# Optimization experiments

Measured on AMD Instinct MI355X. Metric: run time of the kernel, lower is better.

The kernel has to match this reference:

```python
import jax, jax.numpy as jnp
import numpy as np
from jax import lax

NUM_KERNELS = 256
B, C, L = 128, 10, 16384
EPS = 1e-10
NORMALIZE = True
KERNEL_LENGTHS = np.array([7, 9, 11])


def _make_kernel_meta():
    """Deterministic ROCKET-style ragged kernel metadata (static ints)."""
    rng = np.random.default_rng(0)
    lengths = rng.choice(KERNEL_LENGTHS, NUM_KERNELS).astype(np.int64)
    nci = rng.integers(1, C + 1, NUM_KERNELS).astype(np.int64)  # channels per kernel
    channel_indices = np.concatenate(
        [rng.choice(C, int(n), replace=False) for n in nci]).astype(np.int64)
    dilations = np.array(
        [int(2 ** rng.uniform(0.0, np.log2((L - 1) / (l - 1)))) for l in lengths],
        dtype=np.int64)
    paddings = np.array(
        [((l - 1) * d) // 2 if rng.integers(2) else 0 for l, d in zip(lengths, dilations)],
        dtype=np.int64)
    return lengths, nci, channel_indices, dilations, paddings


def setup_inputs() -> dict:
    lengths, nci, channel_indices, dilations, paddings = _make_kernel_meta()
    total_w = int(np.sum(lengths * nci))
    key = jax.random.key(0)
    kx, kw, kb = jax.random.split(key, 3)
    x = jax.random.normal(kx, (B, C, L), dtype=jnp.float32)
    weights = jax.random.normal(kw, (total_w,), dtype=jnp.float32)
    biases = jax.random.uniform(kb, (NUM_KERNELS,), minval=-1.0, maxval=1.0,
                                dtype=jnp.float32)
    return {
        'x': x,
        'weights': weights,
        'biases': biases,
        'lengths': jnp.asarray(lengths),
        'dilations': jnp.asarray(dilations),
        'paddings': jnp.asarray(paddings),
        'num_channel_indices': jnp.asarray(nci),
        'channel_indices': jnp.asarray(channel_indices),
    }


def reference(x, weights, biases, lengths, dilations, paddings,
              num_channel_indices, channel_indices):
    # Ragged metadata must be static (defines per-kernel shapes).
    lengths = np.asarray(lengths)
    dilations = np.asarray(dilations)
    paddings = np.asarray(paddings)
    nci = np.asarray(num_channel_indices)
    channel_indices = np.asarray(channel_indices)
    windices = np.concatenate([[0], np.cumsum(lengths * nci)])
    cindices = np.concatenate([[0], np.cumsum(nci)])

    if NORMALIZE:
        mean_ = jnp.mean(x, axis=-1, keepdims=True)
        std_ = jnp.std(x, axis=-1, keepdims=True, ddof=1)  # torch unbiased std
        x = (x - mean_) / (std_ + EPS)

    ppvs, mxs = [], []
    for k in range(NUM_KERNELS):
        w = weights[windices[k]:windices[k + 1]].reshape(int(nci[k]), int(lengths[k]))
        chans = channel_indices[cindices[k]:cindices[k + 1]]
        px = x[:, chans, :]                       # [B, c_k, L]
        d, p = int(dilations[k]), int(paddings[k])
        yy = lax.conv_general_dilated(
            px, w[None],                          # rhs: [1, c_k, len_k]
            window_strides=(1,), padding=[(p, p)], rhs_dilation=(d,),
            dimension_numbers=('NCH', 'OIH', 'NCH'))[:, 0, :] + biases[k]  # [B, Lout]
        ppvs.append(jnp.mean((yy > 0).astype(x.dtype), axis=-1))
        sm = jax.nn.softmax(yy * 1000.0, axis=-1)  # sharp softmax ~ smooth max
        mxs.append(jnp.sum(sm * yy, axis=-1))

    ppv = jnp.stack(ppvs, axis=1)                 # [B, K]
    mx = jnp.stack(mxs, axis=1)                   # [B, K]
    # interleave: y[:, 2k] = ppv_k, y[:, 2k+1] = mx_k
    return jnp.stack([ppv, mx], axis=2).reshape(x.shape[0], 2 * NUM_KERNELS)
```

## Files before the change

### kernel.cpp

```cpp
#include <hip/hip_runtime.h>

#define NK 256
#define BB 128
#define CC 10
#define LL 16384
#define EPSV 1e-10f
#define GS2 15
#define XW 1792
#define WROW 12

__device__ __forceinline__ void block_finish(int cnt, float mx,
                                             float* rm, int* rc,
                                             int Lout, float* out, int b, int k) {
    int tid = threadIdx.x;
    for (int off = 32; off; off >>= 1) {
        mx = fmaxf(mx, __shfl_down(mx, off));
        cnt += __shfl_down(cnt, off);
    }
    int wv = tid >> 6, ln = tid & 63;
    if (ln == 0) { rm[wv] = mx; rc[wv] = cnt; }
    __syncthreads();
    if (tid == 0) {
#pragma unroll
        for (int i = 1; i < 4; ++i) { mx = fmaxf(mx, rm[i]); cnt += rc[i]; }
        size_t o = (size_t)b * (2 * NK) + 2 * k;
        out[o] = (float)cnt / (float)Lout;
        out[o + 1] = mx;
    }
}

__global__ __launch_bounds__(256) void stats_kernel(const float* __restrict__ x,
                                                    float* __restrict__ wsf) {
    int row = blockIdx.x;
    const float4* x4 = (const float4*)(x + (size_t)row * LL);
    int tid = threadIdx.x;
    float s = 0.f, s2 = 0.f;
    for (int i = tid; i < LL / 4; i += 256) {
        float4 v = x4[i];
        s += v.x + v.y + v.z + v.w;
        s2 += v.x * v.x + v.y * v.y + v.z * v.z + v.w * v.w;
    }
    for (int off = 32; off; off >>= 1) {
        s += __shfl_down(s, off);
        s2 += __shfl_down(s2, off);
    }
    __shared__ float as_[4], as2_[4];
    int wv = tid >> 6, ln = tid & 63;
    if (ln == 0) { as_[wv] = s; as2_[wv] = s2; }
    __syncthreads();
    if (tid == 0) {
        float S = as_[0] + as_[1] + as_[2] + as_[3];
        float S2 = as2_[0] + as2_[1] + as2_[2] + as2_[3];
        float mean = S / (float)LL;
        float var = (S2 - (float)LL * mean * mean) / (float)(LL - 1);
        var = fmaxf(var, 0.f);
        float inv = 1.f / (sqrtf(var) + EPSV);
        wsf[row] = inv;
        wsf[1280 + row] = -mean * inv;
    }
}

__global__ __launch_bounds__(256) void prefix_kernel(const int* __restrict__ lengths,
                                                     const int* __restrict__ ncis,
                                                     int* __restrict__ wbase,
                                                     int* __restrict__ cbase) {
    __shared__ int s1[NK], s2[NK];
    int k = threadIdx.x;
    int v1 = lengths[k] * ncis[k];
    int v2 = ncis[k];
    s1[k] = v1; s2[k] = v2;
    for (int off = 1; off < NK; off <<= 1) {
        __syncthreads();
        int a = (k >= off) ? s1[k - off] : 0;
        int b = (k >= off) ? s2[k - off] : 0;
        __syncthreads();
        s1[k] += a; s2[k] += b;
    }
    __syncthreads();
    wbase[k] = s1[k] - v1;
    cbase[k] = s2[k] - v2;
}

template <int LEN>
__device__ __forceinline__ void conv_S(
    const float* __restrict__ x, float* __restrict__ xw,
    const float* __restrict__ wsmR, const float* __restrict__ wsmS,
    const int* __restrict__ choff, const float* __restrict__ cinv,
    const float* __restrict__ csh,
    int d, int ms, int Lout, int nci, float biasE, float biasI,
    int wu, int lane, int& cnt, float& mx) {
    constexpr int W = GS2 + LEN - 1;
    const int qpt = 64 / d;
    const int MT = qpt * GS2;
    const int stot = d * (MT + LEN - 1);
    const int nit4 = (stot + 3 + 255) >> 8;
    const int nitS = (stot + 3 + 63) >> 6;
    const int Qmax = (Lout + d - 1) / d;
    const int nqt = (Qmax + MT - 1) / MT;
    int qi = lane / d, rho = lane - qi * d;
    bool act = qi < qpt;
    int a0 = act ? qi * GS2 * d + rho : 0;
    float rv[28];

    for (int j = wu; j < nqt; j += 4) {
        int qt = j * MT;
        int tb = (qt - ms) * d;
        int off = tb & 3, base = tb - off;
        bool interior = (base >= 0) && (base + (nit4 << 8) <= LL);
        float acc[GS2];
#pragma unroll
        for (int g = 0; g < GS2; ++g) acc[g] = 0.f;

        if (interior) {
            {
                const float* xp = x + choff[0] + base + 4 * lane;
#pragma unroll
                for (int it = 0; it < 7; ++it)
                    if (it < nit4) *(float4*)&rv[4 * it] = *(const float4*)(xp + (it << 8));
            }
            for (int ci = 0; ci < nci; ++ci) {
#pragma unroll
                for (int it = 0; it < 7; ++it)
                    if (it < nit4) *(float4*)&xw[4 * lane + (it << 8)] = *(const float4*)&rv[4 * it];
                if (ci + 1 < nci) {
                    const float* xp = x + choff[ci + 1] + base + 4 * lane;
#pragma unroll
                    for (int it = 0; it < 7; ++it)
                        if (it < nit4) *(float4*)&rv[4 * it] = *(const float4*)(xp + (it << 8));
                }
                float wreg[WROW];
                const float4* wv4 = (const float4*)&wsmS[ci * WROW];
#pragma unroll
                for (int u = 0; u < (LEN + 3) / 4; ++u) {
                    float4 w4 = wv4[u];
                    wreg[4 * u + 0] = w4.x; wreg[4 * u + 1] = w4.y;
                    wreg[4 * u + 2] = w4.z; wreg[4 * u + 3] = w4.w;
                }
                float win[W];
                int a = off + a0;
#pragma unroll
                for (int i = 0; i < W; ++i) { win[i] = xw[a]; a += d; }
                __builtin_amdgcn_s_setprio(1);
#pragma unroll
                for (int jj = 0; jj < LEN; ++jj)
#pragma unroll
                    for (int g = 0; g < GS2; ++g)
                        acc[g] = fmaf(wreg[jj], win[g + jj], acc[g]);
                __builtin_amdgcn_s_setprio(0);
            }
        } else {
            {
                const float* xc = x + choff[0];
#pragma unroll
                for (int it = 0; it < 26; ++it)
                    if (it < nitS) {
                        int t = base + (it << 6) + lane;
                        t = t < 0 ? 0 : (t > LL - 1 ? LL - 1 : t);
                        rv[it] = xc[t];
                    }
            }
            for (int ci = 0; ci < nci; ++ci) {
                float inv = cinv[ci], sh = csh[ci];
#pragma unroll
                for (int it = 0; it < 26; ++it)
                    if (it < nitS) {
                        int t = base + (it << 6) + lane;
                        float v = ((unsigned)t < (unsigned)LL) ? fmaf(rv[it], inv, sh) : 0.f;
                        xw[(it << 6) + lane] = v;
                    }
                if (ci + 1 < nci) {
                    const float* xc = x + choff[ci + 1];
#pragma unroll
                    for (int it = 0; it < 26; ++it)
                        if (it < nitS) {
                            int t = base + (it << 6) + lane;
                            t = t < 0 ? 0 : (t > LL - 1 ? LL - 1 : t);
                            rv[it] = xc[t];
                        }
                }
                float wreg[WROW];
                const float4* wv4 = (const float4*)&wsmR[ci * WROW];
#pragma unroll
                for (int u = 0; u < (LEN + 3) / 4; ++u) {
                    float4 w4 = wv4[u];
                    wreg[4 * u + 0] = w4.x; wreg[4 * u + 1] = w4.y;
                    wreg[4 * u + 2] = w4.z; wreg[4 * u + 3] = w4.w;
                }
                float win[W];
                int a = off + a0;
#pragma unroll
                for (int i = 0; i < W; ++i) { win[i] = xw[a]; a += d; }
                __builtin_amdgcn_s_setprio(1);
#pragma unroll
                for (int jj = 0; jj < LEN; ++jj)
#pragma unroll
                    for (int g = 0; g < GS2; ++g)
                        acc[g] = fmaf(wreg[jj], win[g + jj], acc[g]);
                __builtin_amdgcn_s_setprio(0);
            }
        }

        float bt = interior ? biasI : biasE;
        if (act) {
            int qb = qt + qi * GS2;
            if ((qb + GS2) * d <= Lout) {
                float am = acc[0];
#pragma unroll
                for (int g = 1; g < GS2; ++g) am = fmaxf(am, acc[g]);
                mx = fmaxf(mx, am + bt);
                float nb = -bt;
#pragma unroll
                for (int g = 0; g < GS2; ++g) cnt += (acc[g] > nb) ? 1 : 0;
            } else {
#pragma unroll
                for (int g = 0; g < GS2; ++g) {
                    int t = (qb + g) * d + rho;
                    if (t < Lout) {
                        float y = acc[g] + bt;
                        cnt += (y > 0.f) ? 1 : 0;
                        mx = fmaxf(mx, y);
                    }
                }
            }
        }
    }
}

template <int LEN, int GG>
__device__ __forceinline__ void conv_T(
    const float* __restrict__ x,
    const float* __restrict__ wsmR, const float* __restrict__ wsmS,
    const int* __restrict__ choff, const float* __restrict__ cinv,
    const float* __restrict__ csh,
    int d, int ms, int Lout, int nci, float biasE, float biasI,
    int wu, int lane, int& cnt, float& mx) {
    constexpr int M = GG + LEN - 1;
    const int Qmax = (Lout + d - 1) / d;
    const int nqt = (Qmax + GG - 1) / GG;
    const int NT = d * nqt;

    for (int f0 = wu * 64; f0 < NT; f0 += 256) {
        int f = f0 + lane;
        bool active = f < NT;
        int fc = active ? f : NT - 1;
        unsigned qi = (unsigned)fc / (unsigned)d;
        int rho = fc - (int)qi * d;
        int qb0 = (int)qi * GG;
        int tl = (qb0 - ms) * d + rho;
        bool laneInt = (tl >= 0) && (tl + (M - 1) * d < LL);
        bool interior = __all(laneInt);
        float acc[GG];
#pragma unroll
        for (int g = 0; g < GG; ++g) acc[g] = 0.f;

        float rA[M], rB[M];

        if (interior) {
            {
                const float* xc = x + choff[0];
                int t = tl;
#pragma unroll
                for (int m = 0; m < M; ++m) { rA[m] = xc[t]; t += d; }
            }
            int ci = 0;
            while (true) {
                if (ci + 1 < nci) {
                    const float* xc = x + choff[ci + 1];
                    int t = tl;
#pragma unroll
                    for (int m = 0; m < M; ++m) { rB[m] = xc[t]; t += d; }
                }
                {
                    float wreg[WROW];
                    const float4* wv4 = (const float4*)&wsmS[ci * WROW];
#pragma unroll
                    for (int u = 0; u < (LEN + 3) / 4; ++u) {
                        float4 w4 = wv4[u];
                        wreg[4 * u + 0] = w4.x; wreg[4 * u + 1] = w4.y;
                        wreg[4 * u + 2] = w4.z; wreg[4 * u + 3] = w4.w;
                    }
                    __builtin_amdgcn_s_setprio(1);
#pragma unroll
                    for (int jj = 0; jj < LEN; ++jj)
#pragma unroll
                        for (int g = 0; g < GG; ++g)
                            acc[g] = fmaf(wreg[jj], rA[g + jj], acc[g]);
                    __builtin_amdgcn_s_setprio(0);
                }
                ++ci; if (ci >= nci) break;
                if (ci + 1 < nci) {
                    const float* xc = x + choff[ci + 1];
                    int t = tl;
#pragma unroll
                    for (int m = 0; m < M; ++m) { rA[m] = xc[t]; t += d; }
                }
                {
                    float wreg[WROW];
                    const float4* wv4 = (const float4*)&wsmS[ci * WROW];
#pragma unroll
                    for (int u = 0; u < (LEN + 3) / 4; ++u) {
                        float4 w4 = wv4[u];
                        wreg[4 * u + 0] = w4.x; wreg[4 * u + 1] = w4.y;
                        wreg[4 * u + 2] = w4.z; wreg[4 * u + 3] = w4.w;
                    }
                    __builtin_amdgcn_s_setprio(1);
#pragma unroll
                    for (int jj = 0; jj < LEN; ++jj)
#pragma unroll
                        for (int g = 0; g < GG; ++g)
                            acc[g] = fmaf(wreg[jj], rB[g + jj], acc[g]);
                    __builtin_amdgcn_s_setprio(0);
                }
                ++ci; if (ci >= nci) break;
            }
        } else {
            {
                const float* xc = x + choff[0];
                int t = tl;
#pragma unroll
                for (int m = 0; m < M; ++m) {
                    int tc = t < 0 ? 0 : (t > LL - 1 ? LL - 1 : t);
                    rA[m] = xc[tc]; t += d;
                }
            }
            int ci = 0;
            while (true) {
                if (ci + 1 < nci) {
                    const float* xc = x + choff[ci + 1];
                    int t = tl;
#pragma unroll
                    for (int m = 0; m < M; ++m) {
                        int tc = t < 0 ? 0 : (t > LL - 1 ? LL - 1 : t);
                        rB[m] = xc[tc]; t += d;
                    }
                }
                {
                    float inv = cinv[ci], sh = csh[ci];
                    int t = tl;
#pragma unroll
                    for (int m = 0; m < M; ++m) {
                        rA[m] = ((unsigned)t < (unsigned)LL) ? fmaf(rA[m], inv, sh) : 0.f;
                        t += d;
                    }
                    float wreg[WROW];
                    const float4* wv4 = (const float4*)&wsmR[ci * WROW];
#pragma unroll
                    for (int u = 0; u < (LEN + 3) / 4; ++u) {
                        float4 w4 = wv4[u];
                        wreg[4 * u + 0] = w4.x; wreg[4 * u + 1] = w4.y;
                        wreg[4 * u + 2] = w4.z; wreg[4 * u + 3] = w4.w;
                    }
                    __builtin_amdgcn_s_setprio(1);
#pragma unroll
                    for (int jj = 0; jj < LEN; ++jj)
#pragma unroll
                        for (int g = 0; g < GG; ++g)
                            acc[g] = fmaf(wreg[jj], rA[g + jj], acc[g]);
                    __builtin_amdgcn_s_setprio(0);
                }
                ++ci; if (ci >= nci) break;
                if (ci + 1 < nci) {
                    const float* xc = x + choff[ci + 1];
                    int t = tl;
#pragma unroll
                    for (int m = 0; m < M; ++m) {
                        int tc = t < 0 ? 0 : (t > LL - 1 ? LL - 1 : t);
                        rA[m] = xc[tc]; t += d;
                    }
                }
                {
                    float inv = cinv[ci], sh = csh[ci];
                    int t = tl;
#pragma unroll
                    for (int m = 0; m < M; ++m) {
                        rB[m] = ((unsigned)t < (unsigned)LL) ? fmaf(rB[m], inv, sh) : 0.f;
                        t += d;
                    }
                    float wreg[WROW];
                    const float4* wv4 = (const float4*)&wsmR[ci * WROW];
#pragma unroll
                    for (int u = 0; u < (LEN + 3) / 4; ++u) {
                        float4 w4 = wv4[u];
                        wreg[4 * u + 0] = w4.x; wreg[4 * u + 1] = w4.y;
                        wreg[4 * u + 2] = w4.z; wreg[4 * u + 3] = w4.w;
                    }
                    __builtin_amdgcn_s_setprio(1);
#pragma unroll
                    for (int jj = 0; jj < LEN; ++jj)
#pragma unroll
                        for (int g = 0; g < GG; ++g)
                            acc[g] = fmaf(wreg[jj], rB[g + jj], acc[g]);
                    __builtin_amdgcn_s_setprio(0);
                }
                ++ci; if (ci >= nci) break;
            }
        }

        float bt = interior ? biasI : biasE;
        if (active) {
            if ((qb0 + GG) * d <= Lout) {
                float am = acc[0];
#pragma unroll
                for (int g = 1; g < GG; ++g) am = fmaxf(am, acc[g]);
                mx = fmaxf(mx, am + bt);
                float nb = -bt;
#pragma unroll
                for (int g = 0; g < GG; ++g) cnt += (acc[g] > nb) ? 1 : 0;
            } else {
#pragma unroll
                for (int g = 0; g < GG; ++g) {
                    int t = (qb0 + g) * d + rho;
                    if (t < Lout) {
                        float y = acc[g] + bt;
                        cnt += (y > 0.f) ? 1 : 0;
                        mx = fmaxf(mx, y);
                    }
                }
            }
        }
    }
}

__global__ __launch_bounds__(256) void conv_kernel(
    const float* __restrict__ x, const float* __restrict__ weights,
    const float* __restrict__ biases,
    const int* __restrict__ lengths, const int* __restrict__ dil,
    const int* __restrict__ pad, const int* __restrict__ ncis,
    const int* __restrict__ chidx,
    const float* __restrict__ wsf, const int* __restrict__ wbase,
    const int* __restrict__ cbase, float* __restrict__ out) {
    int k = blockIdx.x, b = blockIdx.y;
    __shared__ __align__(16) float xl[4 * XW];
    __shared__ __align__(16) float wsmR[CC * WROW];
    __shared__ __align__(16) float wsmS[CC * WROW];
    __shared__ int choff[CC];
    __shared__ float cinv[CC], csh[CC];
    __shared__ float rm[4];
    __shared__ int rc[4];

    int tid = threadIdx.x;
    int len = lengths[k], d = dil[k], p = pad[k], nci = ncis[k];
    int wb = wbase[k], cb = cbase[k];

    if (tid < nci) {
        int ch = chidx[cb + tid];
        choff[tid] = (b * CC + ch) * LL;
        cinv[tid] = wsf[b * CC + ch];
        csh[tid] = wsf[1280 + b * CC + ch];
    }
    __syncthreads();
    for (int i = tid; i < nci * WROW; i += 256) {
        int ci = i / WROW, jj = i - ci * WROW;
        float wv = (jj < len) ? weights[wb + ci * len + jj] : 0.f;
        wsmR[i] = wv;
        wsmS[i] = wv * cinv[ci];
    }
    __syncthreads();

    float csum = 0.f;
    for (int ci = 0; ci < nci; ++ci) {
        float sw = 0.f;
        for (int jj = 0; jj < WROW; ++jj) sw += wsmR[ci * WROW + jj];
        csum += csh[ci] * sw;
    }

    int span = (len - 1) * d;
    int Lout = LL + 2 * p - span;
    int ms = p / d;
    float biasE = biases[k];
    float biasI = biasE + csum;
    int Qmax = (Lout + d - 1) / d;

    int wu = tid >> 6;
    int lane = tid & 63;
    float* xw = xl + wu * XW;
    int cnt = 0;
    float mx = -3.4e38f;

    if (d <= 64) {
        switch (len) {
            case 7:  conv_S<7>(x, xw, wsmR, wsmS, choff, cinv, csh, d, ms, Lout, nci, biasE, biasI, wu, lane, cnt, mx); break;
            case 9:  conv_S<9>(x, xw, wsmR, wsmS, choff, cinv, csh, d, ms, Lout, nci, biasE, biasI, wu, lane, cnt, mx); break;
            default: conv_S<11>(x, xw, wsmR, wsmS, choff, cinv, csh, d, ms, Lout, nci, biasE, biasI, wu, lane, cnt, mx); break;
        }
    } else if (Qmax > 12) {
        switch (len) {
            case 7:  conv_T<7, 16>(x, wsmR, wsmS, choff, cinv, csh, d, ms, Lout, nci, biasE, biasI, wu, lane, cnt, mx); break;
            case 9:  conv_T<9, 16>(x, wsmR, wsmS, choff, cinv, csh, d, ms, Lout, nci, biasE, biasI, wu, lane, cnt, mx); break;
            default: conv_T<11, 16>(x, wsmR, wsmS, choff, cinv, csh, d, ms, Lout, nci, biasE, biasI, wu, lane, cnt, mx); break;
        }
    } else {
        switch (len) {
            case 7:  conv_T<7, 4>(x, wsmR, wsmS, choff, cinv, csh, d, ms, Lout, nci, biasE, biasI, wu, lane, cnt, mx); break;
            case 9:  conv_T<9, 4>(x, wsmR, wsmS, choff, cinv, csh, d, ms, Lout, nci, biasE, biasI, wu, lane, cnt, mx); break;
            default: conv_T<11, 4>(x, wsmR, wsmS, choff, cinv, csh, d, ms, Lout, nci, biasE, biasI, wu, lane, cnt, mx); break;
        }
    }
    block_finish(cnt, mx, rm, rc, Lout, out, b, k);
}

extern "C" void kernel_launch(void* const* d_in, const int* in_sizes, int n_in,
                              void* d_out, int out_size, void* d_ws, size_t ws_size,
                              hipStream_t stream) {
    const float* x = (const float*)d_in[0];
    const float* weights = (const float*)d_in[1];
    const float* biases = (const float*)d_in[2];
    const int* lengths = (const int*)d_in[3];
    const int* dil = (const int*)d_in[4];
    const int* pad = (const int*)d_in[5];
    const int* ncis = (const int*)d_in[6];
    const int* chidx = (const int*)d_in[7];
    float* out = (float*)d_out;

    float* wsf = (float*)d_ws;
    int* wbase = (int*)((char*)d_ws + 2560 * sizeof(float));
    int* cbase = wbase + NK;

    stats_kernel<<<dim3(BB * CC), dim3(256), 0, stream>>>(x, wsf);
    prefix_kernel<<<dim3(1), dim3(256), 0, stream>>>(lengths, ncis, wbase, cbase);
    dim3 grid(NK, BB);
    conv_kernel<<<grid, dim3(256), 0, stream>>>(x, weights, biases, lengths, dil,
                                                pad, ncis, chidx, wsf, wbase,
                                                cbase, out);
}
```

Before: 2.322 ms.

## Deepen prefetch pipeline across tiles and channels, shrink per-thread output groups

conv_S is restructured into a flat software pipeline over (tile, channel) pairs with two register buffers, so loads for the next channel or next tile are issued before the current compute, including across tile boundaries. conv_T's interior path gains triple buffering, prefetching two channels ahead. Output group sizes shrink (GS2 15->11, GG 16->12) along with the LDS window, which lowers register pressure and makes room for the extra buffers. The trade-off is more tiles, each with more halo overhead, in exchange for better latency hiding and possibly higher occupancy.

```diff
diff --git a/kernel.cpp b/kernel.cpp
--- a/kernel.cpp
+++ b/kernel.cpp
@@ -5,8 +5,8 @@
 #define CC 10
 #define LL 16384
 #define EPSV 1e-10f
-#define GS2 15
-#define XW 1792
+#define GS2 11
+#define XW 1536
 #define WROW 12
 
 __device__ __forceinline__ void block_finish(int cnt, float mx,
@@ -100,109 +100,74 @@
     int qi = lane / d, rho = lane - qi * d;
     bool act = qi < qpt;
     int a0 = act ? qi * GS2 * d + rho : 0;
-    float rv[28];
-
-    for (int j = wu; j < nqt; j += 4) {
-        int qt = j * MT;
-        int tb = (qt - ms) * d;
-        int off = tb & 3, base = tb - off;
-        bool interior = (base >= 0) && (base + (nit4 << 8) <= LL);
-        float acc[GS2];
-#pragma unroll
-        for (int g = 0; g < GS2; ++g) acc[g] = 0.f;
-
-        if (interior) {
-            {
-                const float* xp = x + choff[0] + base + 4 * lane;
-#pragma unroll
-                for (int it = 0; it < 7; ++it)
-                    if (it < nit4) *(float4*)&rv[4 * it] = *(const float4*)(xp + (it << 8));
-            }
-            for (int ci = 0; ci < nci; ++ci) {
-#pragma unroll
-                for (int it = 0; it < 7; ++it)
-                    if (it < nit4) *(float4*)&xw[4 * lane + (it << 8)] = *(const float4*)&rv[4 * it];
-                if (ci + 1 < nci) {
-                    const float* xp = x + choff[ci + 1] + base + 4 * lane;
-#pragma unroll
-                    for (int it = 0; it < 7; ++it)
-                        if (it < nit4) *(float4*)&rv[4 * it] = *(const float4*)(xp + (it << 8));
-                }
-                float wreg[WROW];
-                const float4* wv4 = (const float4*)&wsmS[ci * WROW];
-#pragma unroll
-                for (int u = 0; u < (LEN + 3) / 4; ++u) {
-                    float4 w4 = wv4[u];
-                    wreg[4 * u + 0] = w4.x; wreg[4 * u + 1] = w4.y;
-                    wreg[4 * u + 2] = w4.z; wreg[4 * u + 3] = w4.w;
-                }
-                float win[W];
-                int a = off + a0;
-#pragma unroll
-                for (int i = 0; i < W; ++i) { win[i] = xw[a]; a += d; }
-                __builtin_amdgcn_s_setprio(1);
-#pragma unroll
-                for (int jj = 0; jj < LEN; ++jj)
-#pragma unroll
-                    for (int g = 0; g < GS2; ++g)
-                        acc[g] = fmaf(wreg[jj], win[g + jj], acc[g]);
-                __builtin_amdgcn_s_setprio(0);
-            }
+
+    float rvA[24], rvB[24];
+
+    auto tbOf = [&](int j) { return (j * MT - ms) * d; };
+    auto isInt = [&](int tb_) {
+        int base = tb_ - (tb_ & 3);
+        return (base >= 0) && (base + (nit4 << 8) <= LL);
+    };
+    auto pref = [&](float (&rv)[24], int c, int tb_) {
+        int base = tb_ - (tb_ & 3);
+        const float* xc = x + choff[c];
+        if (isInt(tb_)) {
+            const float* xp = xc + base + 4 * lane;
+#pragma unroll
+            for (int it = 0; it < 6; ++it)
+                if (it < nit4) *(float4*)&rv[4 * it] = *(const float4*)(xp + (it << 8));
         } else {
-            {
-                const float* xc = x + choff[0];
-#pragma unroll
-                for (int it = 0; it < 26; ++it)
-                    if (it < nitS) {
-                        int t = base + (it << 6) + lane;
-                        t = t < 0 ? 0 : (t > LL - 1 ? LL - 1 : t);
-                        rv[it] = xc[t];
-                    }
-            }
-            for (int ci = 0; ci < nci; ++ci) {
-                float inv = cinv[ci], sh = csh[ci];
-#pragma unroll
-                for (int it = 0; it < 26; ++it)
-                    if (it < nitS) {
-                        int t = base + (it << 6) + lane;
-                        float v = ((unsigned)t < (unsigned)LL) ? fmaf(rv[it], inv, sh) : 0.f;
-                        xw[(it << 6) + lane] = v;
-                    }
-                if (ci + 1 < nci) {
-                    const float* xc = x + choff[ci + 1];
-#pragma unroll
-                    for (int it = 0; it < 26; ++it)
-                        if (it < nitS) {
-                            int t = base + (it << 6) + lane;
-                            t = t < 0 ? 0 : (t > LL - 1 ? LL - 1 : t);
-                            rv[it] = xc[t];
-                        }
-                }
-                float wreg[WROW];
-                const float4* wv4 = (const float4*)&wsmR[ci * WROW];
-#pragma unroll
-                for (int u = 0; u < (LEN + 3) / 4; ++u) {
-                    float4 w4 = wv4[u];
-                    wreg[4 * u + 0] = w4.x; wreg[4 * u + 1] = w4.y;
-                    wreg[4 * u + 2] = w4.z; wreg[4 * u + 3] = w4.w;
-                }
-                float win[W];
-                int a = off + a0;
-#pragma unroll
-                for (int i = 0; i < W; ++i) { win[i] = xw[a]; a += d; }
-                __builtin_amdgcn_s_setprio(1);
-#pragma unroll
-                for (int jj = 0; jj < LEN; ++jj)
-#pragma unroll
-                    for (int g = 0; g < GS2; ++g)
-                        acc[g] = fmaf(wreg[jj], win[g + jj], acc[g]);
-                __builtin_amdgcn_s_setprio(0);
-            }
-        }
-
-        float bt = interior ? biasI : biasE;
+#pragma unroll
+            for (int it = 0; it < 22; ++it)
+                if (it < nitS) {
+                    int t = base + (it << 6) + lane;
+                    t = t < 0 ? 0 : (t > LL - 1 ? LL - 1 : t);
+                    rv[it] = xc[t];
+                }
+        }
+    };
+    auto wstage = [&](float (&rv)[24], int tb_, float inv, float sh) {
+        int base = tb_ - (tb_ & 3);
+        if (isInt(tb_)) {
+#pragma unroll
+            for (int it = 0; it < 6; ++it)
+                if (it < nit4) *(float4*)&xw[4 * lane + (it << 8)] = *(const float4*)&rv[4 * it];
+        } else {
+#pragma unroll
+            for (int it = 0; it < 22; ++it)
+                if (it < nitS) {
+                    int t = base + (it << 6) + lane;
+                    float v = ((unsigned)t < (unsigned)LL) ? fmaf(rv[it], inv, sh) : 0.f;
+                    xw[(it << 6) + lane] = v;
+                }
+        }
+    };
+    auto compute = [&](int cc, bool I, int off, float (&acc)[GS2]) {
+        const float* wt = I ? wsmS : wsmR;
+        float wreg[WROW];
+        const float4* wv4 = (const float4*)&wt[cc * WROW];
+#pragma unroll
+        for (int u = 0; u < (LEN + 3) / 4; ++u) {
+            float4 w4 = wv4[u];
+            wreg[4 * u + 0] = w4.x; wreg[4 * u + 1] = w4.y;
+            wreg[4 * u + 2] = w4.z; wreg[4 * u + 3] = w4.w;
+        }
+        float win[W];
+        int a = off + a0;
+#pragma unroll
+        for (int i = 0; i < W; ++i) { win[i] = xw[a]; a += d; }
+        __builtin_amdgcn_s_setprio(1);
+#pragma unroll
+        for (int jj = 0; jj < LEN; ++jj)
+#pragma unroll
+            for (int g = 0; g < GS2; ++g)
+                acc[g] = fmaf(wreg[jj], win[g + jj], acc[g]);
+        __builtin_amdgcn_s_setprio(0);
+    };
+    auto epilogue = [&](int jc, bool I, float (&acc)[GS2]) {
+        float bt = I ? biasI : biasE;
         if (act) {
-            int qb = qt + qi * GS2;
+            int qb = jc * MT + qi * GS2;
             if ((qb + GS2) * d <= Lout) {
                 float am = acc[0];
 #pragma unroll
@@ -222,6 +187,47 @@
                     }
                 }
             }
+        }
+    };
+
+    int jc = wu, cc = 0;
+    int jp = wu, cp = 0;
+    auto adv = [&]() { ++cp; if (cp == nci) { cp = 0; jp += 4; } };
+
+    if (jc >= nqt) return;
+
+    pref(rvA, cp, tbOf(jp)); adv();
+    if (jp < nqt) { pref(rvB, cp, tbOf(jp)); adv(); }
+
+    float acc[GS2];
+#pragma unroll
+    for (int g = 0; g < GS2; ++g) acc[g] = 0.f;
+    int tb = tbOf(jc); int off = tb & 3; bool I = isInt(tb);
+
+    while (true) {
+        wstage(rvA, tb, cinv[cc], csh[cc]);
+        if (jp < nqt) { pref(rvA, cp, tbOf(jp)); adv(); }
+        compute(cc, I, off, acc);
+        ++cc;
+        if (cc == nci) {
+            epilogue(jc, I, acc);
+            cc = 0; jc += 4;
+            if (jc >= nqt) break;
+#pragma unroll
+            for (int g = 0; g < GS2; ++g) acc[g] = 0.f;
+            tb = tbOf(jc); off = tb & 3; I = isInt(tb);
+        }
+        wstage(rvB, tb, cinv[cc], csh[cc]);
+        if (jp < nqt) { pref(rvB, cp, tbOf(jp)); adv(); }
+        compute(cc, I, off, acc);
+        ++cc;
+        if (cc == nci) {
+            epilogue(jc, I, acc);
+            cc = 0; jc += 4;
+            if (jc >= nqt) break;
+#pragma unroll
+            for (int g = 0; g < GS2; ++g) acc[g] = 0.f;
+            tb = tbOf(jc); off = tb & 3; I = isInt(tb);
         }
     }
 }
@@ -253,145 +259,76 @@
 #pragma unroll
         for (int g = 0; g < GG; ++g) acc[g] = 0.f;
 
-        float rA[M], rB[M];
+        float rA[M], rB[M], rC[M];
+
+        auto fmaW = [&](float (&r)[M], int c, const float* wt) {
+            float wreg[WROW];
+            const float4* wv4 = (const float4*)&wt[c * WROW];
+#pragma unroll
+            for (int u = 0; u < (LEN + 3) / 4; ++u) {
+                float4 w4 = wv4[u];
+                wreg[4 * u + 0] = w4.x; wreg[4 * u + 1] = w4.y;
+                wreg[4 * u + 2] = w4.z; wreg[4 * u + 3] = w4.w;
+            }
+            __builtin_amdgcn_s_setprio(1);
+#pragma unroll
+            for (int jj = 0; jj < LEN; ++jj)
+#pragma unroll
+                for (int g = 0; g < GG; ++g)
+                    acc[g] = fmaf(wreg[jj], r[g + jj], acc[g]);
+            __builtin_amdgcn_s_setprio(0);
+        };
 
         if (interior) {
-            {
-                const float* xc = x + choff[0];
+            auto ldI = [&](float (&r)[M], int c) {
+                const float* xc = x + choff[c];
                 int t = tl;
 #pragma unroll
-                for (int m = 0; m < M; ++m) { rA[m] = xc[t]; t += d; }
-            }
+                for (int m = 0; m < M; ++m) { r[m] = xc[t]; t += d; }
+            };
+            ldI(rA, 0);
+            if (nci > 1) ldI(rB, 1);
             int ci = 0;
             while (true) {
-                if (ci + 1 < nci) {
-                    const float* xc = x + choff[ci + 1];
-                    int t = tl;
-#pragma unroll
-                    for (int m = 0; m < M; ++m) { rB[m] = xc[t]; t += d; }
-                }
-                {
-                    float wreg[WROW];
-                    const float4* wv4 = (const float4*)&wsmS[ci * WROW];
-#pragma unroll
-                    for (int u = 0; u < (LEN + 3) / 4; ++u) {
-                        float4 w4 = wv4[u];
-                        wreg[4 * u + 0] = w4.x; wreg[4 * u + 1] = w4.y;
-                        wreg[4 * u + 2] = w4.z; wreg[4 * u + 3] = w4.w;
-                    }
-                    __builtin_amdgcn_s_setprio(1);
-#pragma unroll
-                    for (int jj = 0; jj < LEN; ++jj)
-#pragma unroll
-                        for (int g = 0; g < GG; ++g)
-                            acc[g] = fmaf(wreg[jj], rA[g + jj], acc[g]);
-                    __builtin_amdgcn_s_setprio(0);
-                }
+                if (ci + 2 < nci) ldI(rC, ci + 2);
+                fmaW(rA, ci, wsmS);
                 ++ci; if (ci >= nci) break;
-                if (ci + 1 < nci) {
-                    const float* xc = x + choff[ci + 1];
-                    int t = tl;
-#pragma unroll
-                    for (int m = 0; m < M; ++m) { rA[m] = xc[t]; t += d; }
-                }
-                {
-                    float wreg[WROW];
-                    const float4* wv4 = (const float4*)&wsmS[ci * WROW];
-#pragma unroll
-                    for (int u = 0; u < (LEN + 3) / 4; ++u) {
-                        float4 w4 = wv4[u];
-                        wreg[4 * u + 0] = w4.x; wreg[4 * u + 1] = w4.y;
-                        wreg[4 * u + 2] = w4.z; wreg[4 * u + 3] = w4.w;
-                    }
-                    __builtin_amdgcn_s_setprio(1);
-#pragma unroll
-                    for (int jj = 0; jj < LEN; ++jj)
-#pragma unroll
-                        for (int g = 0; g < GG; ++g)
-                            acc[g] = fmaf(wreg[jj], rB[g + jj], acc[g]);
-                    __builtin_amdgcn_s_setprio(0);
-                }
+                if (ci + 2 < nci) ldI(rA, ci + 2);
+                fmaW(rB, ci, wsmS);
+                ++ci; if (ci >= nci) break;
+                if (ci + 2 < nci) ldI(rB, ci + 2);
+                fmaW(rC, ci, wsmS);
                 ++ci; if (ci >= nci) break;
             }
         } else {
-            {
-                const float* xc = x + choff[0];
+            auto ldE = [&](float (&r)[M], int c) {
+                const float* xc = x + choff[c];
                 int t = tl;
 #pragma unroll
                 for (int m = 0; m < M; ++m) {
                     int tc = t < 0 ? 0 : (t > LL - 1 ? LL - 1 : t);
-                    rA[m] = xc[tc]; t += d;
-                }
-            }
+                    r[m] = xc[tc]; t += d;
+                }
+            };
+            auto nrm = [&](float (&r)[M], int c) {
+                float inv = cinv[c], sh = csh[c];
+                int t = tl;
+#pragma unroll
+                for (int m = 0; m < M; ++m) {
+                    r[m] = ((unsigned)t < (unsigned)LL) ? fmaf(r[m], inv, sh) : 0.f;
+                    t += d;
+                }
+            };
+            ldE(rA, 0);
             int ci = 0;
             while (true) {
-                if (ci + 1 < nci) {
-                    const float* xc = x + choff[ci + 1];
-                    int t = tl;
-#pragma unroll
-                    for (int m = 0; m < M; ++m) {
-                        int tc = t < 0 ? 0 : (t > LL - 1 ? LL - 1 : t);
-                        rB[m] = xc[tc]; t += d;
-                    }
-                }
-                {
-                    float inv = cinv[ci], sh = csh[ci];
-                    int t = tl;
-#pragma unroll
-                    for (int m = 0; m < M; ++m) {
-                        rA[m] = ((unsigned)t < (unsigned)LL) ? fmaf(rA[m], inv, sh) : 0.f;
-                        t += d;
-                    }
-                    float wreg[WROW];
-                    const float4* wv4 = (const float4*)&wsmR[ci * WROW];
-#pragma unroll
-                    for (int u = 0; u < (LEN + 3) / 4; ++u) {
-                        float4 w4 = wv4[u];
-                        wreg[4 * u + 0] = w4.x; wreg[4 * u + 1] = w4.y;
-                        wreg[4 * u + 2] = w4.z; wreg[4 * u + 3] = w4.w;
-                    }
-                    __builtin_amdgcn_s_setprio(1);
-#pragma unroll
-                    for (int jj = 0; jj < LEN; ++jj)
-#pragma unroll
-                        for (int g = 0; g < GG; ++g)
-                            acc[g] = fmaf(wreg[jj], rA[g + jj], acc[g]);
-                    __builtin_amdgcn_s_setprio(0);
-                }
+                if (ci + 1 < nci) ldE(rB, ci + 1);
+                nrm(rA, ci);
+                fmaW(rA, ci, wsmR);
                 ++ci; if (ci >= nci) break;
-                if (ci + 1 < nci) {
-                    const float* xc = x + choff[ci + 1];
-                    int t = tl;
-#pragma unroll
-                    for (int m = 0; m < M; ++m) {
-                        int tc = t < 0 ? 0 : (t > LL - 1 ? LL - 1 : t);
-                        rA[m] = xc[tc]; t += d;
-                    }
-                }
-                {
-                    float inv = cinv[ci], sh = csh[ci];
-                    int t = tl;
-#pragma unroll
-                    for (int m = 0; m < M; ++m) {
-                        rB[m] = ((unsigned)t < (unsigned)LL) ? fmaf(rB[m], inv, sh) : 0.f;
-                        t += d;
-                    }
-                    float wreg[WROW];
-                    const float4* wv4 = (const float4*)&wsmR[ci * WROW];
-#pragma unroll
-                    for (int u = 0; u < (LEN + 3) / 4; ++u) {
-                        float4 w4 = wv4[u];
-                        wreg[4 * u + 0] = w4.x; wreg[4 * u + 1] = w4.y;
-                        wreg[4 * u + 2] = w4.z; wreg[4 * u + 3] = w4.w;
-                    }
-                    __builtin_amdgcn_s_setprio(1);
-#pragma unroll
-                    for (int jj = 0; jj < LEN; ++jj)
-#pragma unroll
-                        for (int g = 0; g < GG; ++g)
-                            acc[g] = fmaf(wreg[jj], rB[g + jj], acc[g]);
-                    __builtin_amdgcn_s_setprio(0);
-                }
+                if (ci + 1 < nci) ldE(rA, ci + 1);
+                nrm(rB, ci);
+                fmaW(rB, ci, wsmR);
                 ++ci; if (ci >= nci) break;
             }
         }
@@ -485,9 +422,9 @@
         }
     } else if (Qmax > 12) {
         switch (len) {
-            case 7:  conv_T<7, 16>(x, wsmR, wsmS, choff, cinv, csh, d, ms, Lout, nci, biasE, biasI, wu, lane, cnt, mx); break;
-            case 9:  conv_T<9, 16>(x, wsmR, wsmS, choff, cinv, csh, d, ms, Lout, nci, biasE, biasI, wu, lane, cnt, mx); break;
-            default: conv_T<11, 16>(x, wsmR, wsmS, choff, cinv, csh, d, ms, Lout, nci, biasE, biasI, wu, lane, cnt, mx); break;
+            case 7:  conv_T<7, 12>(x, wsmR, wsmS, choff, cinv, csh, d, ms, Lout, nci, biasE, biasI, wu, lane, cnt, mx); break;
+            case 9:  conv_T<9, 12>(x, wsmR, wsmS, choff, cinv, csh, d, ms, Lout, nci, biasE, biasI, wu, lane, cnt, mx); break;
+            default: conv_T<11, 12>(x, wsmR, wsmS, choff, cinv, csh, d, ms, Lout, nci, biasE, biasI, wu, lane, cnt, mx); break;
         }
     } else {
         switch (len) {
```

New measurement: 5.665 ms. 2.44x slower.
